# Kernel tuning notes

Measured on AMD Instinct MI355X. Metric: run time of the kernel, lower is better.

## Reference

```python
import jax, jax.numpy as jnp
import numpy as np

EPS = 1e-5
NUM_HEADS = 3


def _ln(x, g, b):
    m = jnp.mean(x, axis=-1, keepdims=True)
    v = jnp.mean((x - m) ** 2, axis=-1, keepdims=True)
    return (x - m) * jax.lax.rsqrt(v + EPS) * g + b


def setup_inputs() -> dict:
    key = jax.random.key(0)
    ks = jax.random.split(key, 8)
    Bn, N, C = 256, 197, 192           # graph nodes, tokens per node, embed_dim
    E = 1024                           # edges
    hid = int(C * 4.0)                 # mlp hidden
    def w(k, shape, fan_in):
        return (jax.random.normal(k, shape, jnp.float32) / np.sqrt(fan_in)).astype(jnp.float32)
    return {
        "x": jax.random.normal(ks[0], (Bn, N, C), jnp.float32),
        "egde": jax.random.randint(ks[1], (2, E), 0, Bn),
        "norm1_g": jnp.ones((C,), jnp.float32),
        "norm1_b": jnp.zeros((C,), jnp.float32),
        "qkv_w": w(ks[2], (3 * C, C), C),          # Linear(dim, 3*dim, bias=False)
        "proj_w": w(ks[3], (C, C), C),
        "proj_b": jnp.zeros((C,), jnp.float32),
        "norm2_g": jnp.ones((C,), jnp.float32),
        "norm2_b": jnp.zeros((C,), jnp.float32),
        "fc1_w": w(ks[4], (hid, C), C),
        "fc1_b": jnp.zeros((hid,), jnp.float32),
        "fc2_w": w(ks[5], (C, hid), hid),
        "fc2_b": jnp.zeros((C,), jnp.float32),
    }


def reference(x, egde, norm1_g, norm1_b, qkv_w, proj_w, proj_b,
              norm2_g, norm2_b, fc1_w, fc1_b, fc2_w, fc2_b):
    Bn, N, C = x.shape
    H = NUM_HEADS
    hd = C // H
    scale = hd ** -0.5

    # --- MEConv2 ---
    xn = _ln(x, norm1_g, norm1_b)
    qkv = (xn @ qkv_w.T).reshape(Bn, N, 3, H, hd)
    src, dst = egde[0], egde[1]        # x_j = source, aggregation index = target
    xi = qkv[dst]                      # [E, N, 3, H, hd]
    xj = qkv[src]
    q = xi[:, :, 0]                    # [E, N, H, hd] (from destination)
    v = xi[:, :, 2]                    # note: v comes from x_i, as in the source
    k = xj[:, :, 1]                    # key from source node
    attn = jnp.einsum('enhd,emhd->ehnm', q, k) * scale   # [E, H, N, N]
    attn = jax.nn.softmax(attn, axis=-1)
    msg = jnp.einsum('ehnm,emhd->enhd', attn, v).reshape(-1, N, C)
    msg = msg @ proj_w.T + proj_b      # [E, N, C]
    # scatter-mean over destination nodes (empty nodes -> 0, like torch scatter)
    agg = jax.ops.segment_sum(msg, dst, num_segments=Bn)
    cnt = jax.ops.segment_sum(jnp.ones(dst.shape, x.dtype), dst, num_segments=Bn)
    y = agg / jnp.maximum(cnt, 1.0)[:, None, None]

    # --- residual + MLP ---
    x = x + y
    h = _ln(x, norm2_g, norm2_b)
    h = jax.nn.gelu(h @ fc1_w.T + fc1_b, approximate=False)  # torch nn.GELU = exact
    h = h @ fc2_w.T + fc2_b
    return x + h
```

## Files before the change

### kernel.cpp

```cpp
#include <hip/hip_runtime.h>
#include <hip/hip_bf16.h>
#include <cstddef>


typedef __attribute__((ext_vector_type(8))) short bf8_t;
typedef __attribute__((ext_vector_type(4))) float f4_t;

#define GLOBAL_AS __attribute__((address_space(1)))
#define LDS_AS    __attribute__((address_space(3)))

__device__ __forceinline__ float bf2f(unsigned short u) {
  union { unsigned int i; float f; } x; x.i = ((unsigned int)u) << 16; return x.f;
}
__device__ __forceinline__ unsigned short f2bf(float f) {
  unsigned int u = __builtin_bit_cast(unsigned int, f);
  u = (u + 0x7FFFu + ((u >> 16) & 1u)) >> 16;
  return (unsigned short)u;
}
__device__ __forceinline__ unsigned int cvt_pk_bf16(float a, float b) {
  unsigned int r;
  asm("v_cvt_pk_bf16_f32 %0, %1, %2" : "=v"(r) : "v"(a), "v"(b));
  return r;
}
__device__ __forceinline__ void gload16(const unsigned short* g, unsigned short* l) {
  __builtin_amdgcn_global_load_lds((const GLOBAL_AS unsigned int*)g,
                                   (LDS_AS unsigned int*)l, 16, 0, 0);
}

__global__ __launch_bounds__(256) void wcvt_kernel(
    const float* __restrict__ qkvw, const float* __restrict__ projw,
    const float* __restrict__ fc1w, const float* __restrict__ fc2w,
    unsigned short* __restrict__ dst) {
  int i = blockIdx.x * 256 + threadIdx.x;
  float v;
  if (i < 110592)      v = qkvw[i];
  else if (i < 147456) v = projw[i - 110592];
  else if (i < 294912) v = fc1w[i - 147456];
  else                 v = fc2w[i - 294912];
  dst[i] = f2bf(v);
}

__global__ __launch_bounds__(256) void ln_bf16_kernel(const float* __restrict__ X,
    const float* __restrict__ g, const float* __restrict__ b,
    unsigned short* __restrict__ Y) {
  int row = blockIdx.x * 4 + (threadIdx.x >> 6);
  int lane = threadIdx.x & 63;
  const float* xr = X + (size_t)row * 192;
  float v0 = xr[lane], v1 = xr[lane + 64], v2 = xr[lane + 128];
  float s = v0 + v1 + v2, ss = v0 * v0 + v1 * v1 + v2 * v2;
#pragma unroll
  for (int o = 32; o > 0; o >>= 1) { s += __shfl_xor(s, o, 64); ss += __shfl_xor(ss, o, 64); }
  float mean = s * (1.f / 192.f);
  float var = ss * (1.f / 192.f) - mean * mean;
  float r = rsqrtf(var + 1e-5f);
  unsigned short* yr = Y + (size_t)row * 192;
  yr[lane]       = f2bf((v0 - mean) * r * g[lane]       + b[lane]);
  yr[lane + 64]  = f2bf((v1 - mean) * r * g[lane + 64]  + b[lane + 64]);
  yr[lane + 128] = f2bf((v2 - mean) * r * g[lane + 128] + b[lane + 128]);
}

template<int MODE, int NK>
__global__ __launch_bounds__(256) void gemm_bf16(
    const unsigned short* __restrict__ A, const unsigned short* __restrict__ W,
    const float* __restrict__ bias, const float* __restrict__ xres,
    const int* __restrict__ cntg, void* __restrict__ Cout,
    unsigned short* __restrict__ Cvt, int ldc) {
  constexpr int LDA = 208;
  __shared__ unsigned short As[128 * LDA];
  __shared__ unsigned short Ws[64 * LDA];
  const int tid = threadIdx.x;
  const int m0 = blockIdx.x * 128, n0 = blockIdx.y * 64;
  const int wave = tid >> 6, lane = tid & 63;
  const int mfrag = lane & 15, quad = lane >> 4;
  const int K = NK * 192;

  f4_t acc[2][4];
#pragma unroll
  for (int i = 0; i < 2; ++i)
#pragma unroll
    for (int j = 0; j < 4; ++j) acc[i][j] = (f4_t){0.f, 0.f, 0.f, 0.f};

  for (int kc = 0; kc < NK; ++kc) {
    __syncthreads();
    for (int it = wave; it < 78; it += 4) {
      if (it < 52) {
        int idx = it * 64 + lane;
        int r = idx / 26, c = idx % 26;
        int c8 = min(c * 8, 184);
        gload16(A + (size_t)(m0 + r) * K + kc * 192 + c8, As + it * 512);
      } else {
        int idx = (it - 52) * 64 + lane;
        int r = idx / 26, c = idx % 26;
        int c8 = min(c * 8, 184);
        gload16(W + (size_t)(n0 + r) * K + kc * 192 + c8, Ws + (it - 52) * 512);
      }
    }
    __syncthreads();
#pragma unroll
    for (int ks = 0; ks < 6; ++ks) {
      bf8_t a0 = *(const bf8_t*)(As + (wave * 32 + mfrag) * LDA + ks * 32 + quad * 8);
      bf8_t a1 = *(const bf8_t*)(As + (wave * 32 + 16 + mfrag) * LDA + ks * 32 + quad * 8);
#pragma unroll
      for (int nt = 0; nt < 4; ++nt) {
        bf8_t bf = *(const bf8_t*)(Ws + (nt * 16 + mfrag) * LDA + ks * 32 + quad * 8);
        acc[0][nt] = __builtin_amdgcn_mfma_f32_16x16x32_bf16(a0, bf, acc[0][nt], 0, 0, 0);
        acc[1][nt] = __builtin_amdgcn_mfma_f32_16x16x32_bf16(a1, bf, acc[1][nt], 0, 0, 0);
      }
    }
  }

#pragma unroll
  for (int mt = 0; mt < 2; ++mt)
#pragma unroll
    for (int nt = 0; nt < 4; ++nt)
#pragma unroll
      for (int reg = 0; reg < 4; ++reg) {
        int row = m0 + wave * 32 + mt * 16 + quad * 4 + reg;
        int col = n0 + nt * 16 + mfrag;
        float v = acc[mt][nt][reg];
        if constexpr (MODE == 0) {
          if (col < 384) {
            ((unsigned short*)Cout)[(size_t)row * 384 + col] = f2bf(v);
          } else {
            int cc = col - 384, hh = cc >> 6, dd = cc & 63;
            int bb = row / 197, tt = row - bb * 197;
            Cvt[((size_t)(bb * 3 + hh) * 64 + dd) * 200 + tt] = f2bf(v);
          }
        } else if constexpr (MODE == 2) {
          v += bias[col];
          v = 0.5f * v * (1.f + erff(v * 0.70710678118654752f));
          ((unsigned short*)Cout)[(size_t)row * ldc + col] = f2bf(v);
        } else {
          v += bias[col] + xres[(size_t)row * 192 + col];
          ((float*)Cout)[(size_t)row * ldc + col] = v;
        }
      }
}

__global__ __launch_bounds__(256) void proj_ln_kernel(
    const unsigned short* __restrict__ A,
    const unsigned short* __restrict__ W,
    const float* __restrict__ bias,
    const float* __restrict__ xres,
    const int* __restrict__ cntg,
    const float* __restrict__ g2, const float* __restrict__ b2,
    float* __restrict__ outF,
    unsigned short* __restrict__ xnout) {
  constexpr int LDA = 208;
  __shared__ unsigned short As[128 * LDA];
  __shared__ unsigned short Ws[64 * LDA];
  const int tid = threadIdx.x;
  const int m0 = blockIdx.x * 128;
  const int wave = tid >> 6, lane = tid & 63;
  const int mfrag = lane & 15, quad = lane >> 4;

  f4_t acc[3][2][4];
#pragma unroll
  for (int nc = 0; nc < 3; ++nc)
#pragma unroll
    for (int i = 0; i < 2; ++i)
#pragma unroll
      for (int j = 0; j < 4; ++j) acc[nc][i][j] = (f4_t){0.f, 0.f, 0.f, 0.f};

  for (int it = wave; it < 52; it += 4) {
    int idx = it * 64 + lane;
    int r = idx / 26, c = idx % 26;
    int c8 = min(c * 8, 184);
    gload16(A + (size_t)(m0 + r) * 192 + c8, As + it * 512);
  }

  for (int nc = 0; nc < 3; ++nc) {
    if (nc > 0) __syncthreads();
    for (int it = wave; it < 26; it += 4) {
      int idx = it * 64 + lane;
      int r = idx / 26, c = idx % 26;
      int c8 = min(c * 8, 184);
      gload16(W + (size_t)(nc * 64 + r) * 192 + c8, Ws + it * 512);
    }
    __syncthreads();
#pragma unroll
    for (int ks = 0; ks < 6; ++ks) {
      bf8_t a0 = *(const bf8_t*)(As + (wave * 32 + mfrag) * LDA + ks * 32 + quad * 8);
      bf8_t a1 = *(const bf8_t*)(As + (wave * 32 + 16 + mfrag) * LDA + ks * 32 + quad * 8);
#pragma unroll
      for (int nt = 0; nt < 4; ++nt) {
        bf8_t bf = *(const bf8_t*)(Ws + (nt * 16 + mfrag) * LDA + ks * 32 + quad * 8);
        acc[nc][0][nt] = __builtin_amdgcn_mfma_f32_16x16x32_bf16(a0, bf, acc[nc][0][nt], 0, 0, 0);
        acc[nc][1][nt] = __builtin_amdgcn_mfma_f32_16x16x32_bf16(a1, bf, acc[nc][1][nt], 0, 0, 0);
      }
    }
  }

  float pb[12], pg[12], pbb[12];
#pragma unroll
  for (int nc = 0; nc < 3; ++nc)
#pragma unroll
    for (int nt = 0; nt < 4; ++nt) {
      int col = nc * 64 + nt * 16 + mfrag;
      pb[nc * 4 + nt] = bias[col];
      pg[nc * 4 + nt] = g2[col];
      pbb[nc * 4 + nt] = b2[col];
    }

#pragma unroll
  for (int mt = 0; mt < 2; ++mt)
#pragma unroll
    for (int reg = 0; reg < 4; ++reg) {
      const int row = m0 + wave * 32 + mt * 16 + quad * 4 + reg;
      const int cn = cntg[row / 197];
      const float rc = (cn > 0) ? 1.f / (float)cn : 0.f;
      float vv[12];
      float s = 0.f, ss = 0.f;
#pragma unroll
      for (int nc = 0; nc < 3; ++nc)
#pragma unroll
        for (int nt = 0; nt < 4; ++nt) {
          int col = nc * 64 + nt * 16 + mfrag;
          float v = (cn > 0) ? acc[nc][mt][nt][reg] * rc + pb[nc * 4 + nt] : 0.f;
          v += xres[(size_t)row * 192 + col];
          vv[nc * 4 + nt] = v;
          s += v;
          ss += v * v;
        }
#pragma unroll
      for (int off = 1; off < 16; off <<= 1) {
        s += __shfl_xor(s, off, 64);
        ss += __shfl_xor(ss, off, 64);
      }
      const float mean = s * (1.f / 192.f);
      const float var = ss * (1.f / 192.f) - mean * mean;
      const float r = rsqrtf(var + 1e-5f);
#pragma unroll
      for (int nc = 0; nc < 3; ++nc)
#pragma unroll
        for (int nt = 0; nt < 4; ++nt) {
          int col = nc * 64 + nt * 16 + mfrag;
          float v = vv[nc * 4 + nt];
          outF[(size_t)row * 192 + col] = v;
          xnout[(size_t)row * 192 + col] =
              f2bf((v - mean) * r * pg[nc * 4 + nt] + pbb[nc * 4 + nt]);
        }
    }
}

__global__ __launch_bounds__(512) void attnA_kernel(
    const unsigned short* __restrict__ qk, const unsigned short* __restrict__ vtg,
    const int* __restrict__ edge, unsigned short* __restrict__ msgbuf) {
  const int e = blockIdx.x, h = blockIdx.y;
  const int s = edge[e], b = edge[1024 + e];
  __shared__ unsigned short Ks[208 * 72];
  __shared__ unsigned short Vt[64 * 232];
  __shared__ unsigned short Ps[8][640];
  const int tid = threadIdx.x;
  const int wave = tid >> 6, lane = tid & 63;
  const int mfrag = lane & 15, quad = lane >> 4;

  for (int i = tid; i < 197 * 8; i += 512) {
    int m = i >> 3, c8 = i & 7;
    *(float4*)(Ks + m * 72 + c8 * 8) =
        *(const float4*)(qk + (size_t)(s * 197 + m) * 384 + 192 + h * 64 + c8 * 8);
  }
  for (int i = tid; i < 64 * 25; i += 512) {
    int d = i / 25, c8 = i - d * 25;
    *(float4*)(Vt + d * 232 + c8 * 8) =
        *(const float4*)(vtg + ((size_t)(b * 3 + h) * 64 + d) * 200 + c8 * 8);
  }
  __syncthreads();
  for (int i = tid; i < 64 * 35; i += 512) {
    int d = i / 35, kk = 197 + (i - d * 35);
    Vt[d * 232 + kk] = 0;
  }
  __syncthreads();

  for (int st = wave; st < 13; st += 8) {
    const int m0 = st * 16;
    const size_t qrow = (size_t)(b * 197 + min(m0 + mfrag, 196)) * 384 + h * 64;
    bf8_t a0 = *(const bf8_t*)(qk + qrow + quad * 8);
    bf8_t a1 = *(const bf8_t*)(qk + qrow + 32 + quad * 8);

    f4_t S[13];
#pragma unroll
    for (int nt = 0; nt < 13; ++nt) {
      bf8_t k0 = *(const bf8_t*)(Ks + (nt * 16 + mfrag) * 72 + quad * 8);
      bf8_t k1 = *(const bf8_t*)(Ks + (nt * 16 + mfrag) * 72 + 32 + quad * 8);
      f4_t z = (f4_t){0.f, 0.f, 0.f, 0.f};
      z = __builtin_amdgcn_mfma_f32_16x16x32_bf16(a0, k0, z, 0, 0, 0);
      S[nt] = __builtin_amdgcn_mfma_f32_16x16x32_bf16(a1, k1, z, 0, 0, 0);
    }

#pragma unroll
    for (int reg = 0; reg < 4; ++reg)
      S[12][reg] = (mfrag < 5) ? S[12][reg] : -1e30f;

    float mx[4] = {-1e30f, -1e30f, -1e30f, -1e30f};
#pragma unroll
    for (int nt = 0; nt < 13; ++nt)
#pragma unroll
      for (int reg = 0; reg < 4; ++reg) mx[reg] = fmaxf(mx[reg], S[nt][reg]);
#pragma unroll
    for (int off = 1; off < 16; off <<= 1)
#pragma unroll
      for (int reg = 0; reg < 4; ++reg) mx[reg] = fmaxf(mx[reg], __shfl_xor(mx[reg], off, 64));

    constexpr float CEXP = 0.18033688011112042f;
    float sum[4] = {0.f, 0.f, 0.f, 0.f};
#pragma unroll
    for (int nt = 0; nt < 13; ++nt)
#pragma unroll
      for (int reg = 0; reg < 4; ++reg) {
        float p = exp2f((S[nt][reg] - mx[reg]) * CEXP);
        S[nt][reg] = p;
        sum[reg] += p;
      }
#pragma unroll
    for (int off = 1; off < 16; off <<= 1)
#pragma unroll
      for (int reg = 0; reg < 4; ++reg) sum[reg] += __shfl_xor(sum[reg], off, 64);
    float inv[4];
#pragma unroll
    for (int reg = 0; reg < 4; ++reg) inv[reg] = __builtin_amdgcn_rcpf(sum[reg]);

    f4_t o[4];
#pragma unroll
    for (int dt = 0; dt < 4; ++dt) o[dt] = (f4_t){0.f, 0.f, 0.f, 0.f};
    unsigned short* buf = Ps[wave];
#pragma unroll
    for (int kt = 0; kt < 7; ++kt) {
#pragma unroll
      for (int reg = 0; reg < 4; ++reg) {
        float p0 = S[kt * 2][reg];
        float p1 = (kt * 2 + 1 < 13) ? S[kt * 2 + 1][reg] : 0.f;
        unsigned int u = cvt_pk_bf16(p0, p1);
        buf[(quad * 4 + reg) * 40 + mfrag]      = (unsigned short)u;
        buf[(quad * 4 + reg) * 40 + 16 + mfrag] = (unsigned short)(u >> 16);
      }
      bf8_t pf = *(const bf8_t*)(buf + mfrag * 40 + quad * 8);
#pragma unroll
      for (int dt = 0; dt < 4; ++dt) {
        bf8_t vf = *(const bf8_t*)(Vt + (dt * 16 + mfrag) * 232 + kt * 32 + quad * 8);
        o[dt] = __builtin_amdgcn_mfma_f32_16x16x32_bf16(pf, vf, o[dt], 0, 0, 0);
      }
    }

#pragma unroll
    for (int dt = 0; dt < 4; dt += 2)
#pragma unroll
      for (int reg = 0; reg < 4; ++reg) {
        int q = m0 + quad * 4 + reg;
        unsigned int u = cvt_pk_bf16(o[dt][reg] * inv[reg], o[dt + 1][reg] * inv[reg]);
        if (q < 197) {
          size_t base = (size_t)e * 37824 + q * 192 + h * 64 + dt * 16 + mfrag;
          msgbuf[base]      = (unsigned short)u;
          msgbuf[base + 16] = (unsigned short)(u >> 16);
        }
      }
  }
}

__global__ __launch_bounds__(256) void aggregate_kernel(
    const unsigned short* __restrict__ msgbuf, const int* __restrict__ edge,
    unsigned short* __restrict__ agg, int* __restrict__ cntg) {
  const int b = blockIdx.x, chunk = blockIdx.y;
  __shared__ int list[1024];
  __shared__ int lc;
  const int tid = threadIdx.x;
  if (tid == 0) lc = 0;
  __syncthreads();
  for (int e = tid; e < 1024; e += 256)
    if (edge[1024 + e] == b) { int p = atomicAdd(&lc, 1); list[p] = e; }
  __syncthreads();
  const int cnt = lc;
  if (chunk == 0 && tid == 0) cntg[b] = cnt;
  const int base = chunk * 9456;
  for (int i8 = tid; i8 < 1182; i8 += 256) {
    int i = base + i8 * 8;
    float sum[8];
#pragma unroll
    for (int kk = 0; kk < 8; ++kk) sum[kk] = 0.f;
    for (int j = 0; j < cnt; ++j) {
      float4 t = *(const float4*)(msgbuf + (size_t)list[j] * 37824 + i);
      const unsigned short* u = (const unsigned short*)&t;
#pragma unroll
      for (int kk = 0; kk < 8; ++kk) sum[kk] += bf2f(u[kk]);
    }
    unsigned short o[8];
#pragma unroll
    for (int kk = 0; kk < 8; ++kk) o[kk] = f2bf(sum[kk]);
    *(float4*)(agg + (size_t)b * 37824 + i) = *(const float4*)o;
  }
}

extern "C" void kernel_launch(void* const* d_in, const int* in_sizes, int n_in,
                              void* d_out, int out_size, void* d_ws, size_t ws_size,
                              hipStream_t stream) {
  const float* x      = (const float*)d_in[0];
  const int*   edge   = (const int*)d_in[1];
  const float* n1g    = (const float*)d_in[2];
  const float* n1b    = (const float*)d_in[3];
  const float* qkv_w  = (const float*)d_in[4];
  const float* proj_w = (const float*)d_in[5];
  const float* proj_b = (const float*)d_in[6];
  const float* n2g    = (const float*)d_in[7];
  const float* n2b    = (const float*)d_in[8];
  const float* fc1_w  = (const float*)d_in[9];
  const float* fc1_b  = (const float*)d_in[10];
  const float* fc2_w  = (const float*)d_in[11];
  const float* fc2_b  = (const float*)d_in[12];
  float* out = (float*)d_out;

  char* ws = (char*)d_ws;
  unsigned short* msgbuf = (unsigned short*)ws;
  unsigned short* h1     = (unsigned short*)ws;
  unsigned short* qk     = (unsigned short*)(ws + 77463552);
  unsigned short* xn     = (unsigned short*)(ws + 116195328);
  unsigned short* agg    = (unsigned short*)(ws + 135561216);
  unsigned short* vtg    = (unsigned short*)(ws + 154927104);
  unsigned short* wqkv   = (unsigned short*)(ws + 174587904);
  unsigned short* wproj  = (unsigned short*)(ws + 174809088);
  unsigned short* wfc1   = (unsigned short*)(ws + 174882816);
  unsigned short* wfc2   = (unsigned short*)(ws + 175177728);
  int*            cntg   = (int*)           (ws + 175472640);

  dim3 blk(256);
  wcvt_kernel<<<dim3(1728), blk, 0, stream>>>(qkv_w, proj_w, fc1_w, fc2_w, wqkv);

  ln_bf16_kernel<<<dim3(12608), blk, 0, stream>>>(x, n1g, n1b, xn);
  gemm_bf16<0, 1><<<dim3(394, 9), blk, 0, stream>>>(xn, wqkv, nullptr, nullptr, nullptr, qk, vtg, 384);
  attnA_kernel<<<dim3(1024, 3), dim3(512), 0, stream>>>(qk, vtg, edge, msgbuf);
  aggregate_kernel<<<dim3(256, 4), blk, 0, stream>>>(msgbuf, edge, agg, cntg);
  proj_ln_kernel<<<dim3(394), blk, 0, stream>>>(agg, wproj, proj_b, x, cntg, n2g, n2b, out, xn);
  gemm_bf16<2, 1><<<dim3(394, 12), blk, 0, stream>>>(xn, wfc1, fc1_b, nullptr, nullptr, h1, nullptr, 768);
  gemm_bf16<3, 4><<<dim3(394, 3), blk, 0, stream>>>(h1, wfc2, fc2_b, out, nullptr, out, nullptr, 192);
}
```

Baseline: 449.2 us.

## Fuse fc1+GELU and fc2 GEMMs into a single MLP kernel

Replaces the two separate MLP GEMM launches with one kernel that computes the fc1 output in 64-wide hidden chunks. Each chunk gets bias and GELU applied in registers, is staged in LDS, and is immediately multiplied by the matching fc2 slice into persistent accumulators. This removes the global write and read of the bf16 hidden activation (M x 768) and one launch. In exchange each block reloads all weights from global/L2 with synchronisation between phases, uses smaller 64-row tiles, and keeps 12 accumulator vectors per thread, which may limit occupancy.

```diff
diff --git a/kernel.cpp b/kernel.cpp
--- a/kernel.cpp
+++ b/kernel.cpp
@@ -126,15 +126,99 @@
             int bb = row / 197, tt = row - bb * 197;
             Cvt[((size_t)(bb * 3 + hh) * 64 + dd) * 200 + tt] = f2bf(v);
           }
-        } else if constexpr (MODE == 2) {
-          v += bias[col];
-          v = 0.5f * v * (1.f + erff(v * 0.70710678118654752f));
-          ((unsigned short*)Cout)[(size_t)row * ldc + col] = f2bf(v);
-        } else {
-          v += bias[col] + xres[(size_t)row * 192 + col];
-          ((float*)Cout)[(size_t)row * ldc + col] = v;
         }
       }
+}
+
+__global__ __launch_bounds__(256) void mlp_kernel(
+    const unsigned short* __restrict__ xn,
+    const unsigned short* __restrict__ wfc1,
+    const unsigned short* __restrict__ wfc2,
+    const float* __restrict__ b1, const float* __restrict__ b2,
+    float* __restrict__ outF) {
+  __shared__ unsigned short As[64 * 208];
+  __shared__ unsigned short WF[13824];
+  __shared__ unsigned short Hs[64 * 72];
+  const int tid = threadIdx.x;
+  const int m0 = blockIdx.x * 64;
+  const int wave = tid >> 6, lane = tid & 63;
+  const int mfrag = lane & 15, quad = lane >> 4;
+
+  for (int it = wave; it < 26; it += 4) {
+    int idx = it * 64 + lane;
+    int r = idx / 26, c = idx % 26;
+    int c8 = min(c * 8, 184);
+    gload16(xn + (size_t)(m0 + r) * 192 + c8, As + it * 512);
+  }
+
+  f4_t acc2[12];
+#pragma unroll
+  for (int j = 0; j < 12; ++j) acc2[j] = (f4_t){0.f, 0.f, 0.f, 0.f};
+
+  for (int hc = 0; hc < 12; ++hc) {
+    __syncthreads();
+    for (int it = wave; it < 26; it += 4) {
+      int idx = it * 64 + lane;
+      int r = idx / 26, c = idx % 26;
+      int c8 = min(c * 8, 184);
+      gload16(wfc1 + (size_t)(hc * 64 + r) * 192 + c8, WF + it * 512);
+    }
+    __syncthreads();
+
+    f4_t acc1[4];
+#pragma unroll
+    for (int j = 0; j < 4; ++j) acc1[j] = (f4_t){0.f, 0.f, 0.f, 0.f};
+#pragma unroll
+    for (int ks = 0; ks < 6; ++ks) {
+      bf8_t a0 = *(const bf8_t*)(As + (wave * 16 + mfrag) * 208 + ks * 32 + quad * 8);
+#pragma unroll
+      for (int nt = 0; nt < 4; ++nt) {
+        bf8_t bf = *(const bf8_t*)(WF + (nt * 16 + mfrag) * 208 + ks * 32 + quad * 8);
+        acc1[nt] = __builtin_amdgcn_mfma_f32_16x16x32_bf16(a0, bf, acc1[nt], 0, 0, 0);
+      }
+    }
+#pragma unroll
+    for (int nt = 0; nt < 4; ++nt) {
+      float bb = b1[hc * 64 + nt * 16 + mfrag];
+#pragma unroll
+      for (int reg = 0; reg < 4; ++reg) {
+        float v = acc1[nt][reg] + bb;
+        v = 0.5f * v * (1.f + erff(v * 0.70710678118654752f));
+        Hs[(wave * 16 + quad * 4 + reg) * 72 + nt * 16 + mfrag] = f2bf(v);
+      }
+    }
+
+    __syncthreads();
+    for (int it = wave; it < 27; it += 4) {
+      int idx = it * 64 + lane;
+      int r = idx / 9, sg = idx % 9;
+      int sg8 = min(sg * 8, 56);
+      gload16(wfc2 + (size_t)r * 768 + hc * 64 + sg8, WF + it * 512);
+    }
+    __syncthreads();
+
+#pragma unroll
+    for (int ks = 0; ks < 2; ++ks) {
+      bf8_t a0 = *(const bf8_t*)(Hs + (wave * 16 + mfrag) * 72 + ks * 32 + quad * 8);
+#pragma unroll
+      for (int nt = 0; nt < 12; ++nt) {
+        bf8_t bf = *(const bf8_t*)(WF + (nt * 16 + mfrag) * 72 + ks * 32 + quad * 8);
+        acc2[nt] = __builtin_amdgcn_mfma_f32_16x16x32_bf16(a0, bf, acc2[nt], 0, 0, 0);
+      }
+    }
+  }
+
+#pragma unroll
+  for (int nt = 0; nt < 12; ++nt) {
+    float bb = b2[nt * 16 + mfrag];
+#pragma unroll
+    for (int reg = 0; reg < 4; ++reg) {
+      int row = m0 + wave * 16 + quad * 4 + reg;
+      int col = nt * 16 + mfrag;
+      float v = acc2[nt][reg] + bb + outF[(size_t)row * 192 + col];
+      outF[(size_t)row * 192 + col] = v;
+    }
+  }
 }
 
 __global__ __launch_bounds__(256) void proj_ln_kernel(
@@ -410,7 +494,6 @@
 
   char* ws = (char*)d_ws;
   unsigned short* msgbuf = (unsigned short*)ws;
-  unsigned short* h1     = (unsigned short*)ws;
   unsigned short* qk     = (unsigned short*)(ws + 77463552);
   unsigned short* xn     = (unsigned short*)(ws + 116195328);
   unsigned short* agg    = (unsigned short*)(ws + 135561216);
@@ -429,6 +512,5 @@
   attnA_kernel<<<dim3(1024, 3), dim3(512), 0, stream>>>(qk, vtg, edge, msgbuf);
   aggregate_kernel<<<dim3(256, 4), blk, 0, stream>>>(msgbuf, edge, agg, cntg);
   proj_ln_kernel<<<dim3(394), blk, 0, stream>>>(agg, wproj, proj_b, x, cntg, n2g, n2b, out, xn);
-  gemm_bf16<2, 1><<<dim3(394, 12), blk, 0, stream>>>(xn, wfc1, fc1_b, nullptr, nullptr, h1, nullptr, 768);
-  gemm_bf16<3, 4><<<dim3(394, 3), blk, 0, stream>>>(h1, wfc2, fc2_b, out, nullptr, out, nullptr, 192);
-}
+  mlp_kernel<<<dim3(788), blk, 0, stream>>>(xn, wfc1, wfc2, fc1_b, fc2_b, out);
+}
```

Result: faster. 426.4 us (-5.1%).
